# Performance work log

Hardware: AMD Instinct MI355X
Metric: run time of the kernel (lower is better)

The kernel has to match this reference:

```python
import jax, jax.numpy as jnp
import numpy as np

EPS = 1e-6
NEG_CLAMP = -20.0


def setup_inputs() -> dict:
    key = jax.random.key(0)
    kq, kk, kv = jax.random.split(key, 3)
    B, L, H, E = 8, 4096, 16, 64
    queries = jax.random.normal(kq, (B, L, H, E), dtype=jnp.float32)
    keys = jax.random.normal(kk, (B, L, H, E), dtype=jnp.float32)
    values = jax.random.normal(kv, (B, L, H, E), dtype=jnp.float32)
    delta1 = jnp.zeros((), dtype=jnp.float32)  # nn.Parameter(torch.tensor(0.0))
    return {"queries": queries, "keys": keys, "values": values, "delta1": delta1}


def reference(queries, keys, values, delta1):
    # [B,L,H,E] -> [B,H,L,E]
    q = jnp.swapaxes(queries, 1, 2)
    k = jnp.swapaxes(keys, 1, 2)
    v = jnp.swapaxes(values, 1, 2)

    # mapping_fun == 'softmax_learn': clamp negatives to -20, temperature = softplus(delta1)
    temp = jax.nn.softplus(delta1)
    q = jax.nn.softmax(jnp.where(q < 0, NEG_CLAMP, q) / temp, axis=-1)
    k = jax.nn.softmax(jnp.where(k < 0, NEG_CLAMP, k) / temp, axis=-1)

    # kv = sum_l k[...,l,d] v[...,l,e]  -> [B,H,E,E]
    kv = jnp.einsum('bhld,bhle->bhde', k, v)
    # z_l = 1 / (q_l . sum_l k_l)
    k_sum = k.sum(axis=2)  # [B,H,E]
    z = 1.0 / (jnp.einsum('bhld,bhd->bhl', q, k_sum) + EPS)
    # output [B,L,H,E]
    out = jnp.einsum('bhle,bhed,bhl->blhd', q, kv, z)
    return out
```

## Files before the change

### kernel.cpp

```cpp
#include <hip/hip_runtime.h>

#define L_DIM 4096
#define H_DIM 16
#define E_DIM 64
#define BH 128
#define ROWSTRIDE 1024

#define P1_CHUNK 512
#define P2_CHUNK 512

__device__ __forceinline__ float inv_softplus_temp(const float* delta1) {
  return 1.0f / log1pf(__expf(delta1[0]));
}

__global__ __launch_bounds__(256) void p1_kv(
    const float* __restrict__ Kp, const float* __restrict__ Vp,
    const float* __restrict__ delta1,
    float* __restrict__ ws_kv, float* __restrict__ ws_ksum) {
  const int t = threadIdx.x;
  const int bh = blockIdx.y;
  const int b = bh >> 4, h = bh & 15;
  const int lane = t & 63;
  const int w = t >> 6;
  const float inv_temp = inv_softplus_temp(delta1);
  const size_t base = ((size_t)b * L_DIM * H_DIM + h) * E_DIM;
  const int l0 = blockIdx.x * P1_CHUNK;

  __shared__ float sk[16][64];
  __shared__ float sv[16][64];

  const int rsub = lane >> 4;
  const int equad = (lane & 15) << 2;
  const int srow = (w << 2) | rsub;

  const int d0 = (t >> 4) << 2;
  const int e0 = (t & 15) << 2;

  float acc[4][4];
  float ks[4];
#pragma unroll
  for (int i = 0; i < 4; ++i) {
    ks[i] = 0.f;
#pragma unroll
    for (int j = 0; j < 4; ++j) acc[i][j] = 0.f;
  }

  for (int it = 0; it < P1_CHUNK / 16; ++it) {
    const int l = l0 + it * 16 + srow;
    const float4 k4 = *(const float4*)(Kp + base + (size_t)l * ROWSTRIDE + equad);
    const float4 v4 = *(const float4*)(Vp + base + (size_t)l * ROWSTRIDE + equad);
    float ex = __expf((k4.x < 0.f ? -20.f : k4.x) * inv_temp);
    float ey = __expf((k4.y < 0.f ? -20.f : k4.y) * inv_temp);
    float ez = __expf((k4.z < 0.f ? -20.f : k4.z) * inv_temp);
    float ew = __expf((k4.w < 0.f ? -20.f : k4.w) * inv_temp);
    float s = ex + ey + ez + ew;
    s += __shfl_xor(s, 1);
    s += __shfl_xor(s, 2);
    s += __shfl_xor(s, 4);
    s += __shfl_xor(s, 8);
    const float rs = __builtin_amdgcn_rcpf(s);

    __syncthreads();
    *(float4*)&sk[srow][equad] = make_float4(ex * rs, ey * rs, ez * rs, ew * rs);
    *(float4*)&sv[srow][equad] = v4;
    __syncthreads();

#pragma unroll
    for (int rr = 0; rr < 16; ++rr) {
      const float4 kk = *(const float4*)&sk[rr][d0];
      const float4 vv = *(const float4*)&sv[rr][e0];
      const float ka[4] = {kk.x, kk.y, kk.z, kk.w};
      const float va[4] = {vv.x, vv.y, vv.z, vv.w};
#pragma unroll
      for (int i = 0; i < 4; ++i)
#pragma unroll
        for (int j = 0; j < 4; ++j)
          acc[i][j] = fmaf(ka[i], va[j], acc[i][j]);
      if (e0 == 0) {
        ks[0] += ka[0]; ks[1] += ka[1]; ks[2] += ka[2]; ks[3] += ka[3];
      }
    }
  }

  float* kvdst = ws_kv + (size_t)bh * 4096;
#pragma unroll
  for (int i = 0; i < 4; ++i)
#pragma unroll
    for (int j = 0; j < 4; ++j)
      atomicAdd(&kvdst[(d0 + i) * 64 + (e0 + j)], acc[i][j]);
  if (e0 == 0) {
#pragma unroll
    for (int i = 0; i < 4; ++i)
      atomicAdd(&ws_ksum[bh * 64 + d0 + i], ks[i]);
  }
}

__global__ __launch_bounds__(256) void p2_out(
    const float* __restrict__ Qp, const float* __restrict__ delta1,
    const float* __restrict__ ws_kv, const float* __restrict__ ws_ksum,
    float* __restrict__ outp) {
  const int t = threadIdx.x;
  const int bh = blockIdx.y;
  const int b = bh >> 4, h = bh & 15;
  const int lane = t & 63;
  const int w = t >> 6;
  const float inv_temp = inv_softplus_temp(delta1);
  const size_t base = ((size_t)b * L_DIM * H_DIM + h) * E_DIM;
  const int l0 = blockIdx.x * P2_CHUNK;

  const int rsub = lane >> 4;
  const int equad = (lane & 15) << 2;

  float kvcol[64];
#pragma unroll
  for (int e = 0; e < 64; ++e)
    kvcol[e] = ws_kv[(size_t)bh * 4096 + e * 64 + lane];

  const float4 ks4 = *(const float4*)&ws_ksum[bh * 64 + equad];

  __shared__ float sWT[4][64][4];

  for (int it = 0; it < P2_CHUNK / 16; ++it) {
    const int l = l0 + it * 16 + (w << 2) + rsub;
    const float4 q4 = *(const float4*)(Qp + base + (size_t)l * ROWSTRIDE + equad);
    float ex = __expf((q4.x < 0.f ? -20.f : q4.x) * inv_temp);
    float ey = __expf((q4.y < 0.f ? -20.f : q4.y) * inv_temp);
    float ez = __expf((q4.z < 0.f ? -20.f : q4.z) * inv_temp);
    float ew = __expf((q4.w < 0.f ? -20.f : q4.w) * inv_temp);
    float sE = ex + ey + ez + ew;
    float sD = ex * ks4.x + ey * ks4.y + ez * ks4.z + ew * ks4.w;
    sE += __shfl_xor(sE, 1); sD += __shfl_xor(sD, 1);
    sE += __shfl_xor(sE, 2); sD += __shfl_xor(sD, 2);
    sE += __shfl_xor(sE, 4); sD += __shfl_xor(sD, 4);
    sE += __shfl_xor(sE, 8); sD += __shfl_xor(sD, 8);
    const float scale = __builtin_amdgcn_rcpf(sD + 1e-6f * sE);

    __syncthreads();
    sWT[w][equad + 0][rsub] = ex * scale;
    sWT[w][equad + 1][rsub] = ey * scale;
    sWT[w][equad + 2][rsub] = ez * scale;
    sWT[w][equad + 3][rsub] = ew * scale;
    __syncthreads();

    float a0 = 0.f, a1 = 0.f, a2 = 0.f, a3 = 0.f;
#pragma unroll
    for (int e = 0; e < 64; ++e) {
      const float4 wv = *(const float4*)&sWT[w][e][0];
      const float kve = kvcol[e];
      a0 = fmaf(wv.x, kve, a0);
      a1 = fmaf(wv.y, kve, a1);
      a2 = fmaf(wv.z, kve, a2);
      a3 = fmaf(wv.w, kve, a3);
    }

    const size_t ob = base + (size_t)(l0 + it * 16 + (w << 2)) * ROWSTRIDE + lane;
    outp[ob] = a0;
    outp[ob + ROWSTRIDE] = a1;
    outp[ob + 2 * (size_t)ROWSTRIDE] = a2;
    outp[ob + 3 * (size_t)ROWSTRIDE] = a3;
  }
}

extern "C" void kernel_launch(void* const* d_in, const int* in_sizes, int n_in,
                              void* d_out, int out_size, void* d_ws, size_t ws_size,
                              hipStream_t stream) {
  (void)in_sizes; (void)n_in; (void)out_size; (void)ws_size;
  const float* Q = (const float*)d_in[0];
  const float* K = (const float*)d_in[1];
  const float* V = (const float*)d_in[2];
  const float* delta1 = (const float*)d_in[3];
  float* out = (float*)d_out;

  float* ws_kv = (float*)d_ws;
  float* ws_ksum = ws_kv + (size_t)BH * 4096;
  const size_t zero_bytes = ((size_t)BH * 4096 + (size_t)BH * 64) * sizeof(float);
  hipMemsetAsync(d_ws, 0, zero_bytes, stream);

  dim3 blk(256);
  dim3 g1(L_DIM / P1_CHUNK, BH);
  p1_kv<<<g1, blk, 0, stream>>>(K, V, delta1, ws_kv, ws_ksum);
  dim3 g2(L_DIM / P2_CHUNK, BH);
  p2_out<<<g2, blk, 0, stream>>>(Q, delta1, ws_kv, ws_ksum, out);
}
```

Before: 499.7 us.

## Replace atomics with partial-sum reduction and double-buffer K/V staging

The KV-accumulation kernel now processes 32-row stages with double-buffered shared memory and register prefetch of the next stage. Each thread computes an 8x8 outer-product tile, and the per-block partial results are reduced in shared memory and written out as partials. A separate reduce kernel sums those partials, which removes the global atomics and the memset. The output kernel also processes 32 rows per stage with prefetch. In exchange this adds a third launch and extra workspace traffic, and the larger accumulator tile raises register pressure.

```diff
diff --git a/kernel.cpp b/kernel.cpp
--- a/kernel.cpp
+++ b/kernel.cpp
@@ -5,18 +5,25 @@
 #define E_DIM 64
 #define BH 128
 #define ROWSTRIDE 1024
-
-#define P1_CHUNK 512
-#define P2_CHUNK 512
+#define STG 32
 
 __device__ __forceinline__ float inv_softplus_temp(const float* delta1) {
   return 1.0f / log1pf(__expf(delta1[0]));
 }
 
-__global__ __launch_bounds__(256) void p1_kv(
+__device__ __forceinline__ float4 exp_clamp4(float4 x, float it) {
+  float4 r;
+  r.x = __expf((x.x < 0.f ? -20.f : x.x) * it);
+  r.y = __expf((x.y < 0.f ? -20.f : x.y) * it);
+  r.z = __expf((x.z < 0.f ? -20.f : x.z) * it);
+  r.w = __expf((x.w < 0.f ? -20.f : x.w) * it);
+  return r;
+}
+
+__global__ __launch_bounds__(256, 4) void p1_kv(
     const float* __restrict__ Kp, const float* __restrict__ Vp,
     const float* __restrict__ delta1,
-    float* __restrict__ ws_kv, float* __restrict__ ws_ksum) {
+    float* __restrict__ part_kv, float* __restrict__ part_ks) {
   const int t = threadIdx.x;
   const int bh = blockIdx.y;
   const int b = bh >> 4, h = bh & 15;
@@ -24,80 +31,144 @@
   const int w = t >> 6;
   const float inv_temp = inv_softplus_temp(delta1);
   const size_t base = ((size_t)b * L_DIM * H_DIM + h) * E_DIM;
-  const int l0 = blockIdx.x * P1_CHUNK;
-
-  __shared__ float sk[16][64];
-  __shared__ float sv[16][64];
-
-  const int rsub = lane >> 4;
-  const int equad = (lane & 15) << 2;
-  const int srow = (w << 2) | rsub;
-
-  const int d0 = (t >> 4) << 2;
-  const int e0 = (t & 15) << 2;
-
-  float acc[4][4];
-  float ks[4];
-#pragma unroll
-  for (int i = 0; i < 4; ++i) {
-    ks[i] = 0.f;
-#pragma unroll
-    for (int j = 0; j < 4; ++j) acc[i][j] = 0.f;
-  }
-
-  for (int it = 0; it < P1_CHUNK / 16; ++it) {
-    const int l = l0 + it * 16 + srow;
-    const float4 k4 = *(const float4*)(Kp + base + (size_t)l * ROWSTRIDE + equad);
-    const float4 v4 = *(const float4*)(Vp + base + (size_t)l * ROWSTRIDE + equad);
-    float ex = __expf((k4.x < 0.f ? -20.f : k4.x) * inv_temp);
-    float ey = __expf((k4.y < 0.f ? -20.f : k4.y) * inv_temp);
-    float ez = __expf((k4.z < 0.f ? -20.f : k4.z) * inv_temp);
-    float ew = __expf((k4.w < 0.f ? -20.f : k4.w) * inv_temp);
-    float s = ex + ey + ez + ew;
-    s += __shfl_xor(s, 1);
-    s += __shfl_xor(s, 2);
-    s += __shfl_xor(s, 4);
-    s += __shfl_xor(s, 8);
-    const float rs = __builtin_amdgcn_rcpf(s);
-
+  const int chunk = L_DIM / gridDim.x;
+  const int nstage = chunk / STG;
+  const int l0 = blockIdx.x * chunk;
+
+  __shared__ float sk[2][STG][64];
+  __shared__ float sv[2][STG][64];
+
+  const int srow = t >> 4;
+  const int equad = (t & 15) << 2;
+  const int d0 = (lane >> 3) << 3;
+  const int e0 = (lane & 7) << 3;
+
+  float acc[8][8];
+#pragma unroll
+  for (int i = 0; i < 8; ++i)
+#pragma unroll
+    for (int j = 0; j < 8; ++j) acc[i][j] = 0.f;
+  float4 ksacc = make_float4(0.f, 0.f, 0.f, 0.f);
+
+  const float* kbase = Kp + base + equad;
+  const float* vbase = Vp + base + equad;
+
+  float4 ck0, ck1, cv0, cv1;
+  {
+    const size_t r = (size_t)(l0 + srow) * ROWSTRIDE;
+    ck0 = *(const float4*)(kbase + r);
+    ck1 = *(const float4*)(kbase + r + 16 * (size_t)ROWSTRIDE);
+    cv0 = *(const float4*)(vbase + r);
+    cv1 = *(const float4*)(vbase + r + 16 * (size_t)ROWSTRIDE);
+  }
+
+  for (int s = 0; s < nstage; ++s) {
+    const int buf = s & 1;
+    float4 E0 = exp_clamp4(ck0, inv_temp);
+    float4 E1 = exp_clamp4(ck1, inv_temp);
+    float s0 = E0.x + E0.y + E0.z + E0.w;
+    float s1 = E1.x + E1.y + E1.z + E1.w;
+    s0 += __shfl_xor(s0, 1); s1 += __shfl_xor(s1, 1);
+    s0 += __shfl_xor(s0, 2); s1 += __shfl_xor(s1, 2);
+    s0 += __shfl_xor(s0, 4); s1 += __shfl_xor(s1, 4);
+    s0 += __shfl_xor(s0, 8); s1 += __shfl_xor(s1, 8);
+    const float r0 = __builtin_amdgcn_rcpf(s0);
+    const float r1 = __builtin_amdgcn_rcpf(s1);
+    const float4 kt0 = make_float4(E0.x * r0, E0.y * r0, E0.z * r0, E0.w * r0);
+    const float4 kt1 = make_float4(E1.x * r1, E1.y * r1, E1.z * r1, E1.w * r1);
+    ksacc.x += kt0.x + kt1.x;
+    ksacc.y += kt0.y + kt1.y;
+    ksacc.z += kt0.z + kt1.z;
+    ksacc.w += kt0.w + kt1.w;
+    *(float4*)&sk[buf][srow][equad] = kt0;
+    *(float4*)&sk[buf][srow + 16][equad] = kt1;
+    *(float4*)&sv[buf][srow][equad] = cv0;
+    *(float4*)&sv[buf][srow + 16][equad] = cv1;
     __syncthreads();
-    *(float4*)&sk[srow][equad] = make_float4(ex * rs, ey * rs, ez * rs, ew * rs);
-    *(float4*)&sv[srow][equad] = v4;
+    if (s + 1 < nstage) {
+      const size_t r = (size_t)(l0 + (s + 1) * STG + srow) * ROWSTRIDE;
+      ck0 = *(const float4*)(kbase + r);
+      ck1 = *(const float4*)(kbase + r + 16 * (size_t)ROWSTRIDE);
+      cv0 = *(const float4*)(vbase + r);
+      cv1 = *(const float4*)(vbase + r + 16 * (size_t)ROWSTRIDE);
+    }
+#pragma unroll
+    for (int rr = 0; rr < 8; ++rr) {
+      const int row = (w << 3) + rr;
+      const float4 a0 = *(const float4*)&sk[buf][row][d0];
+      const float4 a1 = *(const float4*)&sk[buf][row][d0 + 4];
+      const float4 b0 = *(const float4*)&sv[buf][row][e0];
+      const float4 b1 = *(const float4*)&sv[buf][row][e0 + 4];
+      const float ka[8] = {a0.x, a0.y, a0.z, a0.w, a1.x, a1.y, a1.z, a1.w};
+      const float vb[8] = {b0.x, b0.y, b0.z, b0.w, b1.x, b1.y, b1.z, b1.w};
+#pragma unroll
+      for (int i = 0; i < 8; ++i)
+#pragma unroll
+        for (int j = 0; j < 8; ++j)
+          acc[i][j] = fmaf(ka[i], vb[j], acc[i][j]);
+    }
+  }
+
+  __syncthreads();
+  float* redks = &sv[0][0][0];
+  *(float4*)&redks[srow * 64 + equad] = ksacc;
+  float* red = &sk[0][0][0];
+  for (int ww = 0; ww < 4; ++ww) {
+    if (w == ww) {
+#pragma unroll
+      for (int i = 0; i < 8; ++i) {
+        float* dst = &red[(d0 + i) * 64 + e0];
+        float4 x0 = make_float4(acc[i][0], acc[i][1], acc[i][2], acc[i][3]);
+        float4 x1 = make_float4(acc[i][4], acc[i][5], acc[i][6], acc[i][7]);
+        if (ww != 0) {
+          const float4 y0 = *(const float4*)&dst[0];
+          const float4 y1 = *(const float4*)&dst[4];
+          x0.x += y0.x; x0.y += y0.y; x0.z += y0.z; x0.w += y0.w;
+          x1.x += y1.x; x1.y += y1.y; x1.z += y1.z; x1.w += y1.w;
+        }
+        *(float4*)&dst[0] = x0;
+        *(float4*)&dst[4] = x1;
+      }
+    }
     __syncthreads();
-
-#pragma unroll
-    for (int rr = 0; rr < 16; ++rr) {
-      const float4 kk = *(const float4*)&sk[rr][d0];
-      const float4 vv = *(const float4*)&sv[rr][e0];
-      const float ka[4] = {kk.x, kk.y, kk.z, kk.w};
-      const float va[4] = {vv.x, vv.y, vv.z, vv.w};
-#pragma unroll
-      for (int i = 0; i < 4; ++i)
-#pragma unroll
-        for (int j = 0; j < 4; ++j)
-          acc[i][j] = fmaf(ka[i], va[j], acc[i][j]);
-      if (e0 == 0) {
-        ks[0] += ka[0]; ks[1] += ka[1]; ks[2] += ka[2]; ks[3] += ka[3];
-      }
-    }
-  }
-
-  float* kvdst = ws_kv + (size_t)bh * 4096;
-#pragma unroll
-  for (int i = 0; i < 4; ++i)
-#pragma unroll
-    for (int j = 0; j < 4; ++j)
-      atomicAdd(&kvdst[(d0 + i) * 64 + (e0 + j)], acc[i][j]);
-  if (e0 == 0) {
-#pragma unroll
-    for (int i = 0; i < 4; ++i)
-      atomicAdd(&ws_ksum[bh * 64 + d0 + i], ks[i]);
-  }
-}
-
-__global__ __launch_bounds__(256) void p2_out(
+  }
+  const int pb = blockIdx.y * gridDim.x + blockIdx.x;
+  float* dkv = part_kv + (size_t)pb * 4096;
+#pragma unroll
+  for (int kk = 0; kk < 4; ++kk)
+    *(float4*)&dkv[kk * 1024 + t * 4] = *(const float4*)&red[kk * 1024 + t * 4];
+  if (t < 64) {
+    float sum = 0.f;
+#pragma unroll
+    for (int r = 0; r < 16; ++r) sum += redks[r * 64 + t];
+    part_ks[pb * 64 + t] = sum;
+  }
+}
+
+__global__ __launch_bounds__(256) void p1_reduce(
+    const float* __restrict__ part_kv, const float* __restrict__ part_ks,
+    float* __restrict__ kv, float* __restrict__ ksum, int px) {
+  const int bh = blockIdx.x;
+  const int t = threadIdx.x;
+#pragma unroll 4
+  for (int i = 0; i < 16; ++i) {
+    const int j = i * 256 + t;
+    float s = 0.f;
+    for (int p = 0; p < px; ++p)
+      s += part_kv[(size_t)(bh * px + p) * 4096 + j];
+    kv[(size_t)bh * 4096 + j] = s;
+  }
+  if (t < 64) {
+    float s = 0.f;
+    for (int p = 0; p < px; ++p)
+      s += part_ks[(bh * px + p) * 64 + t];
+    ksum[bh * 64 + t] = s;
+  }
+}
+
+__global__ __launch_bounds__(256, 4) void p2_out(
     const float* __restrict__ Qp, const float* __restrict__ delta1,
-    const float* __restrict__ ws_kv, const float* __restrict__ ws_ksum,
+    const float* __restrict__ kv, const float* __restrict__ ksum,
     float* __restrict__ outp) {
   const int t = threadIdx.x;
   const int bh = blockIdx.y;
@@ -106,79 +177,110 @@
   const int w = t >> 6;
   const float inv_temp = inv_softplus_temp(delta1);
   const size_t base = ((size_t)b * L_DIM * H_DIM + h) * E_DIM;
-  const int l0 = blockIdx.x * P2_CHUNK;
-
-  const int rsub = lane >> 4;
-  const int equad = (lane & 15) << 2;
+  const int chunk = L_DIM / gridDim.x;
+  const int nstage = chunk / STG;
+  const int l0 = blockIdx.x * chunk;
+
+  __shared__ float sw[2][STG][64];
+
+  const int srow = t >> 4;
+  const int equad = (t & 15) << 2;
 
   float kvcol[64];
 #pragma unroll
   for (int e = 0; e < 64; ++e)
-    kvcol[e] = ws_kv[(size_t)bh * 4096 + e * 64 + lane];
-
-  const float4 ks4 = *(const float4*)&ws_ksum[bh * 64 + equad];
-
-  __shared__ float sWT[4][64][4];
-
-  for (int it = 0; it < P2_CHUNK / 16; ++it) {
-    const int l = l0 + it * 16 + (w << 2) + rsub;
-    const float4 q4 = *(const float4*)(Qp + base + (size_t)l * ROWSTRIDE + equad);
-    float ex = __expf((q4.x < 0.f ? -20.f : q4.x) * inv_temp);
-    float ey = __expf((q4.y < 0.f ? -20.f : q4.y) * inv_temp);
-    float ez = __expf((q4.z < 0.f ? -20.f : q4.z) * inv_temp);
-    float ew = __expf((q4.w < 0.f ? -20.f : q4.w) * inv_temp);
-    float sE = ex + ey + ez + ew;
-    float sD = ex * ks4.x + ey * ks4.y + ez * ks4.z + ew * ks4.w;
-    sE += __shfl_xor(sE, 1); sD += __shfl_xor(sD, 1);
-    sE += __shfl_xor(sE, 2); sD += __shfl_xor(sD, 2);
-    sE += __shfl_xor(sE, 4); sD += __shfl_xor(sD, 4);
-    sE += __shfl_xor(sE, 8); sD += __shfl_xor(sD, 8);
-    const float scale = __builtin_amdgcn_rcpf(sD + 1e-6f * sE);
-
+    kvcol[e] = kv[(size_t)bh * 4096 + e * 64 + lane];
+  const float4 ks4 = *(const float4*)&ksum[bh * 64 + equad];
+
+  const float* qbase = Qp + base + equad;
+  float* obase = outp + base;
+
+  float4 cq0, cq1;
+  {
+    const size_t r = (size_t)(l0 + srow) * ROWSTRIDE;
+    cq0 = *(const float4*)(qbase + r);
+    cq1 = *(const float4*)(qbase + r + 16 * (size_t)ROWSTRIDE);
+  }
+
+  for (int s = 0; s < nstage; ++s) {
+    const int buf = s & 1;
+    float4 E0 = exp_clamp4(cq0, inv_temp);
+    float4 E1 = exp_clamp4(cq1, inv_temp);
+    float sE0 = E0.x + E0.y + E0.z + E0.w;
+    float sE1 = E1.x + E1.y + E1.z + E1.w;
+    float sD0 = E0.x * ks4.x + E0.y * ks4.y + E0.z * ks4.z + E0.w * ks4.w;
+    float sD1 = E1.x * ks4.x + E1.y * ks4.y + E1.z * ks4.z + E1.w * ks4.w;
+    sE0 += __shfl_xor(sE0, 1); sD0 += __shfl_xor(sD0, 1);
+    sE1 += __shfl_xor(sE1, 1); sD1 += __shfl_xor(sD1, 1);
+    sE0 += __shfl_xor(sE0, 2); sD0 += __shfl_xor(sD0, 2);
+    sE1 += __shfl_xor(sE1, 2); sD1 += __shfl_xor(sD1, 2);
+    sE0 += __shfl_xor(sE0, 4); sD0 += __shfl_xor(sD0, 4);
+    sE1 += __shfl_xor(sE1, 4); sD1 += __shfl_xor(sD1, 4);
+    sE0 += __shfl_xor(sE0, 8); sD0 += __shfl_xor(sD0, 8);
+    sE1 += __shfl_xor(sE1, 8); sD1 += __shfl_xor(sD1, 8);
+    const float sc0 = __builtin_amdgcn_rcpf(sD0 + 1e-6f * sE0);
+    const float sc1 = __builtin_amdgcn_rcpf(sD1 + 1e-6f * sE1);
+    *(float4*)&sw[buf][srow][equad] =
+        make_float4(E0.x * sc0, E0.y * sc0, E0.z * sc0, E0.w * sc0);
+    *(float4*)&sw[buf][srow + 16][equad] =
+        make_float4(E1.x * sc1, E1.y * sc1, E1.z * sc1, E1.w * sc1);
     __syncthreads();
-    sWT[w][equad + 0][rsub] = ex * scale;
-    sWT[w][equad + 1][rsub] = ey * scale;
-    sWT[w][equad + 2][rsub] = ez * scale;
-    sWT[w][equad + 3][rsub] = ew * scale;
-    __syncthreads();
-
-    float a0 = 0.f, a1 = 0.f, a2 = 0.f, a3 = 0.f;
+    if (s + 1 < nstage) {
+      const size_t r = (size_t)(l0 + (s + 1) * STG + srow) * ROWSTRIDE;
+      cq0 = *(const float4*)(qbase + r);
+      cq1 = *(const float4*)(qbase + r + 16 * (size_t)ROWSTRIDE);
+    }
+    float a[8];
+#pragma unroll
+    for (int r8 = 0; r8 < 8; ++r8) a[r8] = 0.f;
+    const int rb = w << 2;
 #pragma unroll
     for (int e = 0; e < 64; ++e) {
-      const float4 wv = *(const float4*)&sWT[w][e][0];
       const float kve = kvcol[e];
-      a0 = fmaf(wv.x, kve, a0);
-      a1 = fmaf(wv.y, kve, a1);
-      a2 = fmaf(wv.z, kve, a2);
-      a3 = fmaf(wv.w, kve, a3);
-    }
-
-    const size_t ob = base + (size_t)(l0 + it * 16 + (w << 2)) * ROWSTRIDE + lane;
-    outp[ob] = a0;
-    outp[ob + ROWSTRIDE] = a1;
-    outp[ob + 2 * (size_t)ROWSTRIDE] = a2;
-    outp[ob + 3 * (size_t)ROWSTRIDE] = a3;
+      a[0] = fmaf(sw[buf][rb + 0][e], kve, a[0]);
+      a[1] = fmaf(sw[buf][rb + 1][e], kve, a[1]);
+      a[2] = fmaf(sw[buf][rb + 2][e], kve, a[2]);
+      a[3] = fmaf(sw[buf][rb + 3][e], kve, a[3]);
+      a[4] = fmaf(sw[buf][rb + 16][e], kve, a[4]);
+      a[5] = fmaf(sw[buf][rb + 17][e], kve, a[5]);
+      a[6] = fmaf(sw[buf][rb + 18][e], kve, a[6]);
+      a[7] = fmaf(sw[buf][rb + 19][e], kve, a[7]);
+    }
+    const size_t lrow = (size_t)(l0 + s * STG + rb) * ROWSTRIDE + lane;
+    obase[lrow] = a[0];
+    obase[lrow + ROWSTRIDE] = a[1];
+    obase[lrow + 2 * (size_t)ROWSTRIDE] = a[2];
+    obase[lrow + 3 * (size_t)ROWSTRIDE] = a[3];
+    obase[lrow + 16 * (size_t)ROWSTRIDE] = a[4];
+    obase[lrow + 17 * (size_t)ROWSTRIDE] = a[5];
+    obase[lrow + 18 * (size_t)ROWSTRIDE] = a[6];
+    obase[lrow + 19 * (size_t)ROWSTRIDE] = a[7];
   }
 }
 
 extern "C" void kernel_launch(void* const* d_in, const int* in_sizes, int n_in,
                               void* d_out, int out_size, void* d_ws, size_t ws_size,
                               hipStream_t stream) {
-  (void)in_sizes; (void)n_in; (void)out_size; (void)ws_size;
+  (void)in_sizes; (void)n_in; (void)out_size;
   const float* Q = (const float*)d_in[0];
   const float* K = (const float*)d_in[1];
   const float* V = (const float*)d_in[2];
   const float* delta1 = (const float*)d_in[3];
   float* out = (float*)d_out;
 
-  float* ws_kv = (float*)d_ws;
-  float* ws_ksum = ws_kv + (size_t)BH * 4096;
-  const size_t zero_bytes = ((size_t)BH * 4096 + (size_t)BH * 64) * sizeof(float);
-  hipMemsetAsync(d_ws, 0, zero_bytes, stream);
-
-  dim3 blk(256);
-  dim3 g1(L_DIM / P1_CHUNK, BH);
-  p1_kv<<<g1, blk, 0, stream>>>(K, V, delta1, ws_kv, ws_ksum);
-  dim3 g2(L_DIM / P2_CHUNK, BH);
-  p2_out<<<g2, blk, 0, stream>>>(Q, delta1, ws_kv, ws_ksum, out);
-}
+  int px = 8;
+  for (;;) {
+    size_t need = ((size_t)BH * px * 4096 + (size_t)BH * px * 64 +
+                   (size_t)BH * 4096 + (size_t)BH * 64) * sizeof(float);
+    if (need <= ws_size || px == 1) break;
+    px >>= 1;
+  }
+  float* part_kv = (float*)d_ws;
+  float* part_ks = part_kv + (size_t)BH * px * 4096;
+  float* kvf = part_ks + (size_t)BH * px * 64;
+  float* ksf = kvf + (size_t)BH * 4096;
+
+  p1_kv<<<dim3(px, BH), 256, 0, stream>>>(K, V, delta1, part_kv, part_ks);
+  p1_reduce<<<dim3(BH), 256, 0, stream>>>(part_kv, part_ks, kvf, ksf, px);
+  p2_out<<<dim3(8, BH), 256, 0, stream>>>(Q, delta1, kvf, ksf, out);
+}
```

Result: slower. 856.8 us (+71.5%).
